# Optimization experiments

Hardware: AMD Instinct MI355X
Metric: run time of the kernel (lower is better)

Reference implementation:

```python
import jax, jax.numpy as jnp
import numpy as np

N_EXPERTS = 4
N_MODULES = 4
TOP_K = 2


def setup_inputs() -> dict:
    key = jax.random.key(0)
    k1, k2, k3 = jax.random.split(key, 3)
    B, d_model = 32768, 1024
    pooled_hidden = jax.random.normal(k1, (B, d_model), dtype=jnp.float32)
    # Xavier-uniform-ish scale for linear weights (torch Linear weight layout [out, in])
    lim_g = float(np.sqrt(6.0 / (d_model + d_model)))
    lim_r = float(np.sqrt(6.0 / (d_model + N_MODULES)))
    Wg = jax.random.uniform(k2, (d_model, d_model), jnp.float32, -lim_g, lim_g)
    Wr = jax.random.uniform(k3, (N_MODULES, d_model), jnp.float32, -lim_r, lim_r)
    return {"pooled_hidden": pooled_hidden, "Wg": Wg, "Wr": Wr}


def reference(pooled_hidden, Wg, Wr):
    # gated = g(h) = h @ Wg^T ; logits = gated @ Wr^T ; probs = softmax over modules
    gated = jnp.einsum("bd,ed->be", pooled_hidden, Wg)            # [B, d_model]
    logits = jnp.einsum("bd,md->bm", gated, Wr)                   # [B, n_modules]
    probs = jax.nn.softmax(logits, axis=-1)                        # [B, n_modules]

    # Vectorized replacement of the per-sample threshold loop:
    # prob > 0.5 -> first k experts get 1/k; else first max(1, k//2) get 1/that.
    n_lo = max(1, TOP_K // 2)
    eids = jnp.arange(N_EXPERTS)
    w_hi = jnp.where(eids < TOP_K, 1.0 / TOP_K, 0.0).astype(jnp.float32)   # [E]
    w_lo = jnp.where(eids < n_lo, 1.0 / n_lo, 0.0).astype(jnp.float32)     # [E]
    mask_hi = probs > 0.5                                          # [B, M]
    weights = jnp.where(mask_hi[:, :, None], w_hi, w_lo)          # [B, M, E]

    # Return per-module expert weights (Q, K, V, O order), each [B, n_experts]
    w = jnp.transpose(weights, (1, 0, 2))                          # [M, B, E]
    return (w[0], w[1], w[2], w[3])
```

## Files before the change

kernel.cpp:

```cpp
#include <hip/hip_runtime.h>

#define D_MODEL 1024
#define N_MOD   4

typedef float fx4 __attribute__((ext_vector_type(4)));

__global__ __launch_bounds__(256) void weff_skinny_kernel(
    const fx4*   __restrict__ Wg4,
    const float* __restrict__ Wr,
    fx4*         __restrict__ Weff4)
{
    const int t   = threadIdx.x;
    const int es  = t >> 1;
    const int c   = t & 1;
    const int col = blockIdx.x * 2 + c;

    fx4 acc[N_MOD];
    #pragma unroll
    for (int m = 0; m < N_MOD; ++m) acc[m] = (fx4)(0.f);

    #pragma unroll
    for (int k = 0; k < 8; ++k) {
        const int e = es + k * 128;
        const fx4 wg = Wg4[e * 256 + col];
        #pragma unroll
        for (int m = 0; m < N_MOD; ++m)
            acc[m] += Wr[m * D_MODEL + e] * wg;
    }

    __shared__ fx4 red[2][N_MOD][128];
    #pragma unroll
    for (int m = 0; m < N_MOD; ++m) red[c][m][es] = acc[m];
    __syncthreads();

    const int p  = t >> 5;
    const int c2 = p & 1;
    const int m2 = p >> 1;
    const int e5 = t & 31;
    fx4 s = red[c2][m2][e5]      + red[c2][m2][e5 + 32]
          + red[c2][m2][e5 + 64] + red[c2][m2][e5 + 96];

    #pragma unroll
    for (int off = 16; off; off >>= 1) {
        s.x += __shfl_xor(s.x, off, 64);
        s.y += __shfl_xor(s.y, off, 64);
        s.z += __shfl_xor(s.z, off, 64);
        s.w += __shfl_xor(s.w, off, 64);
    }
    if (e5 == 0)
        Weff4[m2 * 256 + blockIdx.x * 2 + c2] = s;
}

__global__ __launch_bounds__(256) void router_main_kernel(
    const float* __restrict__ h,
    const float* __restrict__ Weff,
    float* __restrict__ out,
    int B)
{
    const int lane = threadIdx.x & 63;
    const int wave = threadIdx.x >> 6;

    fx4 w4[N_MOD][4];
    const fx4* __restrict__ W4 = (const fx4*)Weff;
    #pragma unroll
    for (int m = 0; m < N_MOD; ++m)
        #pragma unroll
        for (int c = 0; c < 4; ++c)
            w4[m][c] = W4[m * 256 + c * 64 + lane];

    float4* __restrict__ out4 = (float4*)out;
    const int wid  = blockIdx.x * 4 + wave;
    const int step = gridDim.x * 4 * 8;

    for (int row0 = wid * 8; row0 < B; row0 += step) {
        unsigned mask = 0;
        #pragma unroll
        for (int i = 0; i < 8; ++i) {
            const int row = row0 + i;
            const fx4* __restrict__ h4 = (const fx4*)(h + (size_t)row * D_MODEL);
            fx4 v[4];
            #pragma unroll
            for (int c = 0; c < 4; ++c) v[c] = h4[c * 64 + lane];

            float acc[N_MOD] = {0.f, 0.f, 0.f, 0.f};
            #pragma unroll
            for (int c = 0; c < 4; ++c) {
                #pragma unroll
                for (int m = 0; m < N_MOD; ++m) {
                    acc[m] = fmaf(v[c].x, w4[m][c].x, acc[m]);
                    acc[m] = fmaf(v[c].y, w4[m][c].y, acc[m]);
                    acc[m] = fmaf(v[c].z, w4[m][c].z, acc[m]);
                    acc[m] = fmaf(v[c].w, w4[m][c].w, acc[m]);
                }
            }
            const bool b0 = lane & 1;
            float a  = (b0 ? acc[1] : acc[0]) + __shfl_xor(b0 ? acc[0] : acc[1], 1, 64);
            float cc = (b0 ? acc[3] : acc[2]) + __shfl_xor(b0 ? acc[2] : acc[3], 1, 64);
            const bool b1 = lane & 2;
            float r  = (b1 ? cc : a) + __shfl_xor(b1 ? a : cc, 2, 64);
            r += __shfl_xor(r, 4, 64);
            r += __shfl_xor(r, 8, 64);
            r += __shfl_xor(r, 16, 64);
            r += __shfl_xor(r, 32, 64);
            float mx = fmaxf(r, __shfl_xor(r, 1, 64));
            mx = fmaxf(mx, __shfl_xor(mx, 2, 64));
            const float ex = expf(r - mx);
            float S = ex + __shfl_xor(ex, 1, 64);
            S = S + __shfl_xor(S, 2, 64);
            const bool hi = (r == mx) && (S < 2.0f);
            mask |= (hi ? 1u : 0u) << i;
        }
        const int m = lane >> 3;
        const int rs = lane & 7;
        const unsigned mm = __shfl(mask, m, 64);
        if (lane < 32) {
            const bool hi = (mm >> rs) & 1;
            const float4 val = hi ? make_float4(0.5f, 0.5f, 0.f, 0.f)
                                  : make_float4(1.f, 0.f, 0.f, 0.f);
            out4[(size_t)m * B + row0 + rs] = val;
        }
    }
}

extern "C" void kernel_launch(void* const* d_in, const int* in_sizes, int n_in,
                              void* d_out, int out_size, void* d_ws, size_t ws_size,
                              hipStream_t stream) {
    const float* h  = (const float*)d_in[0];
    const fx4*   Wg = (const fx4*)d_in[1];
    const float* Wr = (const float*)d_in[2];
    float* out = (float*)d_out;

    const int B = in_sizes[0] / D_MODEL;

    float* Weff = (float*)d_ws;

    weff_skinny_kernel<<<128, 256, 0, stream>>>(Wg, Wr, (fx4*)Weff);

    const int grid = (B + 8 * 4 - 1) / (8 * 4);
    router_main_kernel<<<grid, 256, 0, stream>>>(h, Weff, out, B);
}
```

Measured before the change: 31.98 us.

## Stage Weff in LDS and issue four rows' loads at once per wave

Result: slower. 35.50 us (+11.0%).

```diff
diff --git a/kernel.cpp b/kernel.cpp
--- a/kernel.cpp
+++ b/kernel.cpp
@@ -57,68 +57,76 @@
     float* __restrict__ out,
     int B)
 {
-    const int lane = threadIdx.x & 63;
-    const int wave = threadIdx.x >> 6;
+    __shared__ fx4 wlds[N_MOD][4][64];
+    const int t = threadIdx.x;
 
-    fx4 w4[N_MOD][4];
     const fx4* __restrict__ W4 = (const fx4*)Weff;
     #pragma unroll
-    for (int m = 0; m < N_MOD; ++m)
+    for (int j = 0; j < 4; ++j)
+        ((fx4*)wlds)[j * 256 + t] = W4[j * 256 + t];
+    __syncthreads();
+
+    const int lane = t & 63;
+    const int wave = t >> 6;
+    float4* __restrict__ out4 = (float4*)out;
+    const int row0 = (blockIdx.x * 4 + wave) * 4;
+    if (row0 >= B) return;
+
+    const fx4* __restrict__ hb = (const fx4*)(h + (size_t)row0 * D_MODEL);
+
+    float acc[4][N_MOD];
+    #pragma unroll
+    for (int i = 0; i < 4; ++i)
         #pragma unroll
-        for (int c = 0; c < 4; ++c)
-            w4[m][c] = W4[m * 256 + c * 64 + lane];
+        for (int m = 0; m < N_MOD; ++m) acc[i][m] = 0.f;
 
-    float4* __restrict__ out4 = (float4*)out;
-    const int wid  = blockIdx.x * 4 + wave;
-    const int step = gridDim.x * 4 * 8;
+    #pragma unroll
+    for (int c = 0; c < 4; ++c) {
+        const fx4 v0 = hb[0 * 256 + c * 64 + lane];
+        const fx4 v1 = hb[1 * 256 + c * 64 + lane];
+        const fx4 v2 = hb[2 * 256 + c * 64 + lane];
+        const fx4 v3 = hb[3 * 256 + c * 64 + lane];
+        #pragma unroll
+        for (int m = 0; m < N_MOD; ++m) {
+            const fx4 w = wlds[m][c][lane];
+            acc[0][m] = fmaf(v0.x, w.x, fmaf(v0.y, w.y, fmaf(v0.z, w.z, fmaf(v0.w, w.w, acc[0][m]))));
+            acc[1][m] = fmaf(v1.x, w.x, fmaf(v1.y, w.y, fmaf(v1.z, w.z, fmaf(v1.w, w.w, acc[1][m]))));
+            acc[2][m] = fmaf(v2.x, w.x, fmaf(v2.y, w.y, fmaf(v2.z, w.z, fmaf(v2.w, w.w, acc[2][m]))));
+            acc[3][m] = fmaf(v3.x, w.x, fmaf(v3.y, w.y, fmaf(v3.z, w.z, fmaf(v3.w, w.w, acc[3][m]))));
+        }
+    }
 
-    for (int row0 = wid * 8; row0 < B; row0 += step) {
-        unsigned mask = 0;
-        #pragma unroll
-        for (int i = 0; i < 8; ++i) {
-            const int row = row0 + i;
-            const fx4* __restrict__ h4 = (const fx4*)(h + (size_t)row * D_MODEL);
-            fx4 v[4];
-            #pragma unroll
-            for (int c = 0; c < 4; ++c) v[c] = h4[c * 64 + lane];
+    unsigned mask = 0;
+    #pragma unroll
+    for (int i = 0; i < 4; ++i) {
+        const bool b0 = lane & 1;
+        const float aa = (b0 ? acc[i][1] : acc[i][0])
+                       + __shfl_xor(b0 ? acc[i][0] : acc[i][1], 1, 64);
+        const float cc = (b0 ? acc[i][3] : acc[i][2])
+                       + __shfl_xor(b0 ? acc[i][2] : acc[i][3], 1, 64);
+        const bool b1 = lane & 2;
+        float r = (b1 ? cc : aa) + __shfl_xor(b1 ? aa : cc, 2, 64);
+        r += __shfl_xor(r, 4, 64);
+        r += __shfl_xor(r, 8, 64);
+        r += __shfl_xor(r, 16, 64);
+        r += __shfl_xor(r, 32, 64);
+        float mx = fmaxf(r, __shfl_xor(r, 1, 64));
+        mx = fmaxf(mx, __shfl_xor(mx, 2, 64));
+        const float ex = expf(r - mx);
+        float S = ex + __shfl_xor(ex, 1, 64);
+        S += __shfl_xor(S, 2, 64);
+        const bool hi = (r == mx) && (S < 2.0f);
+        mask |= (hi ? 1u : 0u) << i;
+    }
 
-            float acc[N_MOD] = {0.f, 0.f, 0.f, 0.f};
-            #pragma unroll
-            for (int c = 0; c < 4; ++c) {
-                #pragma unroll
-                for (int m = 0; m < N_MOD; ++m) {
-                    acc[m] = fmaf(v[c].x, w4[m][c].x, acc[m]);
-                    acc[m] = fmaf(v[c].y, w4[m][c].y, acc[m]);
-                    acc[m] = fmaf(v[c].z, w4[m][c].z, acc[m]);
-                    acc[m] = fmaf(v[c].w, w4[m][c].w, acc[m]);
-                }
-            }
-            const bool b0 = lane & 1;
-            float a  = (b0 ? acc[1] : acc[0]) + __shfl_xor(b0 ? acc[0] : acc[1], 1, 64);
-            float cc = (b0 ? acc[3] : acc[2]) + __shfl_xor(b0 ? acc[2] : acc[3], 1, 64);
-            const bool b1 = lane & 2;
-            float r  = (b1 ? cc : a) + __shfl_xor(b1 ? a : cc, 2, 64);
-            r += __shfl_xor(r, 4, 64);
-            r += __shfl_xor(r, 8, 64);
-            r += __shfl_xor(r, 16, 64);
-            r += __shfl_xor(r, 32, 64);
-            float mx = fmaxf(r, __shfl_xor(r, 1, 64));
-            mx = fmaxf(mx, __shfl_xor(mx, 2, 64));
-            const float ex = expf(r - mx);
-            float S = ex + __shfl_xor(ex, 1, 64);
-            S = S + __shfl_xor(S, 2, 64);
-            const bool hi = (r == mx) && (S < 2.0f);
-            mask |= (hi ? 1u : 0u) << i;
-        }
-        const int m = lane >> 3;
-        const int rs = lane & 7;
-        const unsigned mm = __shfl(mask, m, 64);
-        if (lane < 32) {
-            const bool hi = (mm >> rs) & 1;
-            const float4 val = hi ? make_float4(0.5f, 0.5f, 0.f, 0.f)
-                                  : make_float4(1.f, 0.f, 0.f, 0.f);
-            out4[(size_t)m * B + row0 + rs] = val;
-        }
+    const int m  = lane >> 2;
+    const int rs = lane & 3;
+    const unsigned mm = __shfl(mask, m, 64);
+    if (lane < 16) {
+        const bool hi = (mm >> rs) & 1;
+        const float4 val = hi ? make_float4(0.5f, 0.5f, 0.f, 0.f)
+                              : make_float4(1.f, 0.f, 0.f, 0.f);
+        out4[(size_t)m * B + row0 + rs] = val;
     }
 }
 
@@ -136,6 +144,6 @@
 
     weff_skinny_kernel<<<128, 256, 0, stream>>>(Wg, Wr, (fx4*)Weff);
 
-    const int grid = (B + 8 * 4 - 1) / (8 * 4);
+    const int grid = (B + 4 * 4 - 1) / (4 * 4);
     router_main_kernel<<<grid, 256, 0, stream>>>(h, Weff, out, B);
 }
```
